# Kernel tuning notes

Hardware: AMD Instinct MI355X
Metric: run time of the kernel (lower is better)

## Reference

```python
import jax, jax.numpy as jnp
import numpy as np

NUM_HEADS = 8
D_HEAD = 64
LN_EPS = 1e-6


def _pad_idx(lengths, max_len):
    # flat indices into a [B*max_len, ...] dense buffer for each packed token
    return np.concatenate([b * max_len + np.arange(int(l)) for b, l in enumerate(lengths)])


def _layer_norm(x, scale, bias):
    mu = jnp.mean(x, axis=-1, keepdims=True)
    var = jnp.mean(jnp.square(x - mu), axis=-1, keepdims=True)
    return (x - mu) * jax.lax.rsqrt(var + LN_EPS) * scale + bias


def setup_inputs() -> dict:
    key = jax.random.key(0)
    ks = jax.random.split(key, 12)
    d_model, d_ff, H, dh = 512, 2048, NUM_HEADS, D_HEAD
    lengths = np.array([128 * (i + 1) for i in range(8)], dtype=np.int64)  # sum = 4608
    total = int(lengths.sum())
    s = 0.02
    return {
        "x": jax.random.normal(ks[0], (total, d_model), jnp.float32),
        "mem": jax.random.normal(ks[1], (total, d_model), jnp.float32),
        "lengths_x": lengths,
        "lengths_mem": lengths.copy(),
        "Wq": jax.random.normal(ks[2], (d_model, H * dh), jnp.float32) * s,
        "Wk": jax.random.normal(ks[3], (d_model, H * dh), jnp.float32) * s,
        "Wv": jax.random.normal(ks[4], (d_model, H * dh), jnp.float32) * s,
        "Wo": jax.random.normal(ks[5], (H * dh, d_model), jnp.float32) * s,
        "ln1_scale": jnp.ones((d_model,), jnp.float32),
        "ln1_bias": jnp.zeros((d_model,), jnp.float32),
        "W1": jax.random.normal(ks[6], (d_model, d_ff), jnp.float32) * s,
        "b1": jnp.zeros((d_ff,), jnp.float32),
        "W2": jax.random.normal(ks[7], (d_ff, d_model), jnp.float32) * s,
        "b2": jnp.zeros((d_model,), jnp.float32),
        "ln2_scale": jnp.ones((d_model,), jnp.float32),
        "ln2_bias": jnp.zeros((d_model,), jnp.float32),
    }


def reference(x, mem, lengths_x, lengths_mem, Wq, Wk, Wv, Wo,
              ln1_scale, ln1_bias, W1, b1, W2, b2, ln2_scale, ln2_bias):
    lx = np.asarray(lengths_x)
    lm = np.asarray(lengths_mem)
    B = lx.shape[0]
    Lx = int(lx.max())
    Lm = int(lm.max())
    H, dh = NUM_HEADS, D_HEAD

    idx_x = _pad_idx(lx, Lx)
    idx_m = _pad_idx(lm, Lm)

    def pad(packed, idx, B, L):
        dense = jnp.zeros((B * L,) + packed.shape[1:], packed.dtype).at[idx].set(packed)
        return dense.reshape((B, L) + packed.shape[1:])

    q = pad((x @ Wq).reshape(-1, H, dh), idx_x, B, Lx)   # [B, Lx, H, dh]
    k = pad((mem @ Wk).reshape(-1, H, dh), idx_m, B, Lm)  # [B, Lm, H, dh]
    v = pad((mem @ Wv).reshape(-1, H, dh), idx_m, B, Lm)

    e = jnp.einsum('bxhd,byhd->bhxy', q, k) / np.sqrt(dh)  # [B, H, Lx, Lm]
    # validity mask: (query pos < len_x) & (key pos < len_mem)
    mask = (np.arange(Lx)[None, :, None] < lx[:, None, None]) & \
           (np.arange(Lm)[None, None, :] < lm[:, None, None])
    mask = jnp.asarray(mask)[:, None, :, :]  # [B, 1, Lx, Lm]
    e = jnp.where(mask, e, jnp.float32(-1e30))  # finite -inf surrogate; identical softmax on valid rows
    alpha = jax.nn.softmax(e, axis=-1)
    out = jnp.einsum('bhxy,byhd->bxhd', alpha, v).reshape(B, Lx, H * dh)
    out = out @ Wo                                  # [B, Lx, d_model]
    out = out.reshape(B * Lx, -1)[idx_x]            # pack back to [total_x, d_model]

    h = _layer_norm(x + out, ln1_scale, ln1_bias)
    ffn = jax.nn.relu(h @ W1 + b1) @ W2 + b2
    return _layer_norm(h + ffn, ln2_scale, ln2_bias)
```

## Files before the change

### kernel.cpp

```cpp
#include <hip/hip_runtime.h>
#include <stdint.h>

typedef short bf8v __attribute__((ext_vector_type(8)));
typedef float f4v  __attribute__((ext_vector_type(4)));
typedef short s8v  __attribute__((ext_vector_type(8)));
typedef short s4v  __attribute__((ext_vector_type(4)));
typedef int   i2v  __attribute__((ext_vector_type(2)));

__device__ __forceinline__ float bf2f(short b){
  unsigned u = ((unsigned)(unsigned short)b) << 16;
  union { unsigned u; float f; } c; c.u = u; return c.f;
}
__device__ __forceinline__ short f2bf(float f){
  union { float f; unsigned u; } c; c.f = f;
  unsigned r = (c.u + 0x7FFFu + ((c.u >> 16) & 1u)) >> 16;
  return (short)r;
}
__device__ __forceinline__ void gload16(const short* g, short* l){
  __builtin_amdgcn_global_load_lds(
      (const __attribute__((address_space(1))) void*)g,
      (__attribute__((address_space(3))) void*)l, 16, 0, 0);
}

__global__ __launch_bounds__(256) void setup_kernel(
    const int* lx, const int* lm, int* meta,
    const float* __restrict__ x, const float* __restrict__ mem,
    short* __restrict__ xb, short* __restrict__ mb, long long n, int nblk_cvt,
    const float* __restrict__ Wq, const float* __restrict__ Wk,
    const float* __restrict__ Wv, const float* __restrict__ Wo,
    const float* __restrict__ W1, const float* __restrict__ W2,
    short* __restrict__ WqT, short* __restrict__ WkT,
    short* __restrict__ WvT, short* __restrict__ WoT,
    short* __restrict__ W1T, short* __restrict__ W2T){
  __shared__ int sjp[9], skvc[8];
  __shared__ float tile[32][33];
  int tid = threadIdx.x;
  int bid = blockIdx.x;

  if (bid == 0){
    if (tid == 0){
      int is64 = ((lx[1] | lx[3] | lx[5] | lx[7]) == 0) ? 1 : 0;
      int ox = 0, om = 0;
      for (int b = 0; b < 8; ++b){
        int a = is64 ? lx[2*b] : lx[b];
        int c = is64 ? lm[2*b] : lm[b];
        meta[b] = a; meta[8+b] = c;
        meta[16+b] = ox; meta[25+b] = om;
        ox += a; om += c;
      }
      meta[24] = ox; meta[33] = om;
      int jp = 0;
      for (int b = 0; b < 8; ++b){
        int Lm_ = meta[8+b];
        int kvc = (Lm_ + 255) / 256; if (kvc > 4) kvc = 4; if (kvc < 1) kvc = 1;
        int clen = (((Lm_ + kvc - 1) / kvc) + 31) & ~31;
        meta[34+b] = kvc; meta[42+b] = clen;
        meta[50+b] = jp;
        sjp[b] = jp; skvc[b] = kvc;
        int qt = (meta[b] + 63) / 64;
        jp += qt * kvc * 8;
      }
      meta[58] = jp;
      sjp[8] = jp;
    }
    __syncthreads();
    int njobs = sjp[8];
    for (int j = tid; j < njobs; j += blockDim.x){
      int b = 0;
      #pragma unroll
      for (int i = 1; i < 8; ++i) if (j >= sjp[i]) b = i;
      int local = j - sjp[b];
      int kvc = skvc[b];
      int h = local & 7;
      int r = local >> 3;
      int c = r % kvc;
      int qt = r / kvc;
      meta[64+j] = b | (h << 4) | (c << 7) | (qt << 11);
    }
    return;
  }

  if (bid <= nblk_cvt){
    long long t = (long long)(bid - 1) * 256 + tid;
    long long i = t * 8;
    const float* s; short* d;
    if (i < n){ s = x + i; d = xb + i; }
    else {
      i -= n; if (i >= n) return;
      s = mem + i; d = mb + i;
    }
    float4 f0 = *(const float4*)s;
    float4 f1 = *(const float4*)(s + 4);
    s8v o;
    o[0]=f2bf(f0.x); o[1]=f2bf(f0.y); o[2]=f2bf(f0.z); o[3]=f2bf(f0.w);
    o[4]=f2bf(f1.x); o[5]=f2bf(f1.y); o[6]=f2bf(f1.z); o[7]=f2bf(f1.w);
    *(s8v*)d = o;
    return;
  }

  int wbid = bid - 1 - nblk_cvt;
  const float* W; short* WT; int K, N, t0;
  if      (wbid <  256){ W=Wq; WT=WqT; K=512;  N=512;  t0=0;    }
  else if (wbid <  512){ W=Wk; WT=WkT; K=512;  N=512;  t0=256;  }
  else if (wbid <  768){ W=Wv; WT=WvT; K=512;  N=512;  t0=512;  }
  else if (wbid < 1024){ W=Wo; WT=WoT; K=512;  N=512;  t0=768;  }
  else if (wbid < 2048){ W=W1; WT=W1T; K=512;  N=2048; t0=1024; }
  else                 { W=W2; WT=W2T; K=2048; N=512;  t0=2048; }
  int lt = wbid - t0;
  int ntn = N / 32;
  int tk = lt / ntn, tn = lt % ntn;
  int r0 = tid >> 5, c = tid & 31;
  #pragma unroll
  for (int i = 0; i < 4; ++i){
    int r = r0 + i*8;
    tile[r][c] = W[(long)(tk*32 + r)*N + tn*32 + c];
  }
  __syncthreads();
  #pragma unroll
  for (int i = 0; i < 4; ++i){
    int r = r0 + i*8;
    WT[(long)(tn*32 + r)*K + tk*32 + c] = f2bf(tile[c][r]);
  }
}

__device__ __forceinline__ void stage_g64(const short* A, const short* Bt,
    long brow, long bcol, int M, int N, int K, int t,
    short* Als, short* Bls){
  int tid = threadIdx.x;
  {
    int cc = tid;
    int row = cc >> 2, slot = cc & 3;
    int cg = slot ^ ((row >> 1) & 3);
    long ar = brow + row; if (ar >= M) ar = M - 1;
    gload16(A + ar*(long)K + t + cg*8, &Als[cc*8]);
  }
  #pragma unroll
  for (int i = 0; i < 2; ++i){
    int cc = i*256 + tid;
    int row = cc >> 2, slot = cc & 3;
    int cg = slot ^ ((row >> 1) & 3);
    long br = bcol + row; if (br >= N) br = N - 1;
    gload16(Bt + br*(long)K + t + cg*8, &Bls[cc*8]);
  }
}

__device__ __forceinline__ void gemm_core64(const short* A, const short* Bt,
    short* __restrict__ Cb, const float* __restrict__ bias,
    int M, int N, int K, int k0, int klen,
    float scale, int relu, int colmajor,
    long brow, long bcol, short* Als, short* Bls){
  int tid = threadIdx.x;
  int lane = tid & 63, w = tid >> 6;
  int wcol = w * 32;
  int l15 = lane & 15, l4 = lane >> 4;

  f4v acc[4][2];
  #pragma unroll
  for (int m = 0; m < 4; ++m)
    #pragma unroll
    for (int n = 0; n < 2; ++n) acc[m][n] = (f4v){0.f,0.f,0.f,0.f};

  int nt = klen / 32;
  stage_g64(A, Bt, brow, bcol, M, N, K, k0, Als, Bls);
  for (int t = 0; t < nt; ++t){
    __syncthreads();
    if (t + 1 < nt)
      stage_g64(A, Bt, brow, bcol, M, N, K, k0 + (t+1)*32,
                Als + ((t+1)&1)*2048, Bls + ((t+1)&1)*4096);
    const short* Ab = Als + (t&1)*2048;
    const short* Bb = Bls + (t&1)*4096;
    bf8v a[4], b[2];
    #pragma unroll
    for (int m = 0; m < 4; ++m){
      int row = m*16 + l15;
      a[m] = *(const bf8v*)&Ab[row*32 + (l4 ^ ((row >> 1) & 3))*8];
    }
    #pragma unroll
    for (int n = 0; n < 2; ++n){
      int row = wcol + n*16 + l15;
      b[n] = *(const bf8v*)&Bb[row*32 + (l4 ^ ((row >> 1) & 3))*8];
    }
    #pragma unroll
    for (int m = 0; m < 4; ++m){
      acc[m][0] = __builtin_amdgcn_mfma_f32_16x16x32_bf16(a[m], b[0], acc[m][0], 0, 0, 0);
      acc[m][1] = __builtin_amdgcn_mfma_f32_16x16x32_bf16(a[m], b[1], acc[m][1], 0, 0, 0);
    }
  }

  #pragma unroll
  for (int m = 0; m < 4; ++m){
    #pragma unroll
    for (int n = 0; n < 2; ++n){
      long col = bcol + wcol + n*16 + l15;
      float bi = (bias != nullptr && col < N) ? bias[col] : 0.f;
      #pragma unroll
      for (int j = 0; j < 4; ++j){
        long row = brow + m*16 + 4*l4 + j;
        if (row < M && col < N){
          float v = acc[m][n][j] * scale + bi;
          if (relu) v = fmaxf(v, 0.f);
          Cb[colmajor ? (col*(long)M + row) : (row*(long)N + col)] = f2bf(v);
        }
      }
    }
  }
}

__global__ __launch_bounds__(256) void gemm64(
    const short* __restrict__ A, const short* __restrict__ Bt,
    short* __restrict__ C, const float* __restrict__ bias,
    int M, int N, int K, int klen, float scale, int relu, int colmajor){
  __shared__ __align__(16) short Als[2*64*32];
  __shared__ __align__(16) short Bls[2*128*32];
  int chunk = blockIdx.z;
  gemm_core64(A, Bt, C + (long)chunk * M * N, bias, M, N, K, chunk*klen, klen,
              scale, relu, colmajor,
              (long)blockIdx.y * 64, (long)blockIdx.x * 128, Als, Bls);
}

__global__ __launch_bounds__(256) void gemm_qkv(
    const short* __restrict__ xb, const short* __restrict__ mb,
    const short* __restrict__ WqT, const short* __restrict__ WkT,
    const short* __restrict__ WvT,
    short* __restrict__ Qb, short* __restrict__ Kbf, short* __restrict__ Vtb,
    int total){
  __shared__ __align__(16) short Als[2*64*32];
  __shared__ __align__(16) short Bls[2*128*32];
  int seg = blockIdx.x >> 2;
  const short* A  = (seg == 0) ? xb : mb;
  const short* Bt = (seg == 0) ? WqT : ((seg == 1) ? WkT : WvT);
  short* C        = (seg == 0) ? Qb  : ((seg == 1) ? Kbf : Vtb);
  float scale     = (seg == 0) ? 0.125f : 1.f;
  int colmajor    = (seg == 2);
  gemm_core64(A, Bt, C, nullptr, total, 512, 512, 0, 512, scale, 0, colmajor,
              (long)blockIdx.y * 64, (long)(blockIdx.x & 3) * 128, Als, Bls);
}

__global__ __launch_bounds__(256) void attn_kernel(
    const short* __restrict__ Q, const short* __restrict__ Kb,
    const short* __restrict__ Vt, short* __restrict__ Ob,
    short* __restrict__ Opart, float* __restrict__ mlpart,
    const int* __restrict__ meta, int total){
  __shared__ __align__(16) short Kls[2][32*64];
  __shared__ __align__(16) short Vls[2][64*32];
  __shared__ __align__(16) short Pls[4][16*32];
  int tid = threadIdx.x;
  int lane = tid & 63, w = tid >> 6;
  int l15 = lane & 15, l4 = lane >> 4;
  int njobs = meta[58];

  for (int j = blockIdx.x; j < njobs; j += gridDim.x){
    int word = meta[64+j];
    int b = word & 15, h = (word >> 4) & 7, c = (word >> 7) & 15, qt = word >> 11;
    int Lx = meta[b], Lm = meta[8+b];
    int ox = meta[16+b], om = meta[25+b];
    int kvc = meta[34+b], clen = meta[42+b];
    int c0 = c * clen;
    int cend = c0 + clen; if (cend > Lm) cend = Lm;
    int nt = (cend - c0 + 31) / 32;
    int qbase = qt*64 + w*16;

    __syncthreads();

    #define ATTN_STAGE(T, BUF)                                                  \
      {                                                                         \
        int kv0_ = c0 + (T)*32;                                                 \
        int kr = tid >> 3, ks_ = tid & 7;                                       \
        int cgk = ks_ ^ (kr & 7);                                               \
        int ktok = kv0_ + kr; if (ktok >= Lm) ktok = Lm - 1;                    \
        gload16(Kb + (long)(om + ktok)*512 + h*64 + cgk*8, &Kls[BUF][tid*8]);   \
        int vr = tid >> 2, vs = tid & 3;                                        \
        int cgv = vs ^ (vr & 3);                                                \
        int vkv = kv0_ + cgv*8; if (vkv + 8 > Lm) vkv = Lm - 8;                 \
        gload16(Vt + (long)(h*64 + vr)*total + om + vkv, &Vls[BUF][tid*8]);     \
      }

    ATTN_STAGE(0, 0)

    int qr = qbase + l15;
    const short* qp = Q + (long)(ox + (qr < Lx ? qr : Lx - 1))*512 + h*64 + l4*8;
    bf8v aq0 = *(const bf8v*)qp;
    bf8v aq1 = *(const bf8v*)(qp + 32);

    float mrun = -1e30f, lrun = 0.f;
    f4v o[4];
    #pragma unroll
    for (int n = 0; n < 4; ++n) o[n] = (f4v){0.f,0.f,0.f,0.f};

    for (int t = 0; t < nt; ++t){
      __syncthreads();
      if (t + 1 < nt) ATTN_STAGE(t+1, (t+1)&1)
      int buf = t & 1;
      int kv0 = c0 + t*32;

      f4v s[2];
      #pragma unroll
      for (int n = 0; n < 2; ++n){
        int krow = n*16 + l15;
        bf8v k0 = *(const bf8v*)&Kls[buf][krow*64 + ((l4    ) ^ (krow & 7))*8];
        bf8v k1 = *(const bf8v*)&Kls[buf][krow*64 + ((4 + l4) ^ (krow & 7))*8];
        f4v z = (f4v){0.f,0.f,0.f,0.f};
        z = __builtin_amdgcn_mfma_f32_16x16x32_bf16(k0, aq0, z, 0, 0, 0);
        z = __builtin_amdgcn_mfma_f32_16x16x32_bf16(k1, aq1, z, 0, 0, 0);
        s[n] = z;
      }
      if (kv0 + 32 > cend){
        #pragma unroll
        for (int n = 0; n < 2; ++n){
          int kvb = kv0 + n*16 + 4*l4;
          #pragma unroll
          for (int jj = 0; jj < 4; ++jj)
            if (kvb + jj >= cend) s[n][jj] = -1e30f;
        }
      }
      float m1 = fmaxf(fmaxf(fmaxf(s[0][0], s[0][1]), fmaxf(s[0][2], s[0][3])),
                       fmaxf(fmaxf(s[1][0], s[1][1]), fmaxf(s[1][2], s[1][3])));
      m1 = fmaxf(m1, __shfl_xor(m1, 16, 64));
      m1 = fmaxf(m1, __shfl_xor(m1, 32, 64));
      float mnew = fmaxf(mrun, m1);
      float sc = __expf(mrun - mnew);
      mrun = mnew;
      float rs = 0.f;
      #pragma unroll
      for (int n = 0; n < 2; ++n)
        #pragma unroll
        for (int jj = 0; jj < 4; ++jj){
          float p = __expf(s[n][jj] - mnew);
          s[n][jj] = p; rs += p;
        }
      rs += __shfl_xor(rs, 16, 64);
      rs += __shfl_xor(rs, 32, 64);
      lrun = lrun * sc + rs;
      #pragma unroll
      for (int n = 0; n < 4; ++n) o[n] *= sc;

      #pragma unroll
      for (int n = 0; n < 2; ++n){
        unsigned r0, r1;
        asm("v_cvt_pk_bf16_f32 %0, %1, %2" : "=v"(r0) : "v"(s[n][0]), "v"(s[n][1]));
        asm("v_cvt_pk_bf16_f32 %0, %1, %2" : "=v"(r1) : "v"(s[n][2]), "v"(s[n][3]));
        i2v pr; pr[0] = (int)r0; pr[1] = (int)r1;
        int cs = (n*4 + l4) ^ ((l15 & 3) << 1);
        *(i2v*)&Pls[w][l15*32 + cs*4] = pr;
      }
      bf8v pb = *(const bf8v*)&Pls[w][l15*32 + (((2*l4) ^ ((l15 & 3) << 1))*4)];

      #pragma unroll
      for (int n2 = 0; n2 < 4; ++n2){
        int vrow = n2*16 + l15;
        bf8v vv = *(const bf8v*)&Vls[buf][vrow*32 + ((l4 ^ (vrow & 3))*8)];
        o[n2] = __builtin_amdgcn_mfma_f32_16x16x32_bf16(vv, pb, o[n2], 0, 0, 0);
      }
    }
    #undef ATTN_STAGE

    if (qr < Lx){
      if (kvc == 1){
        float inv = 1.f / lrun;
        long obase = (long)(ox + qr)*512 + h*64;
        #pragma unroll
        for (int n2 = 0; n2 < 4; ++n2){
          s4v ov;
          #pragma unroll
          for (int jj = 0; jj < 4; ++jj) ov[jj] = f2bf(o[n2][jj] * inv);
          *(s4v*)&Ob[obase + n2*16 + l4*4] = ov;
        }
      } else {
        long slot = ((long)(ox + qr)*8 + h)*4 + c;
        #pragma unroll
        for (int n2 = 0; n2 < 4; ++n2){
          s4v ov;
          #pragma unroll
          for (int jj = 0; jj < 4; ++jj) ov[jj] = f2bf(o[n2][jj]);
          *(s4v*)&Opart[slot*64 + n2*16 + l4*4] = ov;
        }
        if (l4 == 0){
          float2 ml; ml.x = mrun; ml.y = lrun;
          *(float2*)&mlpart[slot*2] = ml;
        }
      }
    }
  }
}

__global__ __launch_bounds__(256) void attn_combine(
    const short* __restrict__ Opart, const float* __restrict__ mlpart,
    short* __restrict__ Ob, const int* __restrict__ meta, int total){
  int w = threadIdx.x >> 6, lane = threadIdx.x & 63;
  int row = blockIdx.x*4 + w;
  if (row >= total) return;
  int b = 0;
  #pragma unroll
  for (int i = 1; i < 8; ++i) if (row >= meta[16+i]) b = i;
  int kvc = meta[34+b];
  if (kvc <= 1) return;
  for (int h = 0; h < 8; ++h){
    long sbase = ((long)row*8 + h)*4;
    float m_ = -1e30f;
    for (int c = 0; c < kvc; ++c) m_ = fmaxf(m_, mlpart[(sbase+c)*2]);
    float num = 0.f, den = 0.f;
    for (int c = 0; c < kvc; ++c){
      float mc = mlpart[(sbase+c)*2];
      float lc = mlpart[(sbase+c)*2 + 1];
      float wgt = __expf(mc - m_);
      num += wgt * bf2f(Opart[(sbase+c)*64 + lane]);
      den += wgt * lc;
    }
    Ob[(long)row*512 + h*64 + lane] = f2bf(num / den);
  }
}

__global__ __launch_bounds__(256) void ln_fuse(
    const float* __restrict__ Af, const short* __restrict__ Ab,
    const short* __restrict__ PartB, int nparts, long pstride,
    const float* __restrict__ bias,
    const float* __restrict__ gamma, const float* __restrict__ beta,
    short* __restrict__ outb, float* __restrict__ outf, int rows){
  int w = threadIdx.x >> 6, lane = threadIdx.x & 63;
  long row = (long)blockIdx.x * 4 + w;
  if (row >= rows) return;
  int c0 = lane * 8;
  long base = row * 512 + c0;
  float v[8];
  if (Af){
    float4 f0 = *(const float4*)(Af + base);
    float4 f1 = *(const float4*)(Af + base + 4);
    v[0]=f0.x; v[1]=f0.y; v[2]=f0.z; v[3]=f0.w;
    v[4]=f1.x; v[5]=f1.y; v[6]=f1.z; v[7]=f1.w;
  } else {
    s8v a = *(const s8v*)(Ab + base);
    #pragma unroll
    for (int j = 0; j < 8; ++j) v[j] = bf2f(a[j]);
  }
  for (int c = 0; c < nparts; ++c){
    s8v pv = *(const s8v*)(PartB + c*pstride + base);
    #pragma unroll
    for (int j = 0; j < 8; ++j) v[j] += bf2f(pv[j]);
  }
  if (bias){
    #pragma unroll
    for (int j = 0; j < 8; ++j) v[j] += bias[c0 + j];
  }
  float sum = 0.f;
  #pragma unroll
  for (int j = 0; j < 8; ++j) sum += v[j];
  #pragma unroll
  for (int m = 1; m < 64; m <<= 1) sum += __shfl_xor(sum, m, 64);
  float mu = sum * (1.f/512.f);
  float q = 0.f;
  #pragma unroll
  for (int j = 0; j < 8; ++j){ float d = v[j] - mu; q += d*d; }
  #pragma unroll
  for (int m = 1; m < 64; m <<= 1) q += __shfl_xor(q, m, 64);
  float rs = rsqrtf(q * (1.f/512.f) + 1e-6f);
  float ov[8];
  #pragma unroll
  for (int j = 0; j < 8; ++j)
    ov[j] = (v[j] - mu) * rs * gamma[c0 + j] + beta[c0 + j];
  if (outb){
    s8v os;
    #pragma unroll
    for (int j = 0; j < 8; ++j) os[j] = f2bf(ov[j]);
    *(s8v*)(outb + base) = os;
  }
  if (outf){
    float4 f0 = {ov[0], ov[1], ov[2], ov[3]};
    float4 f1 = {ov[4], ov[5], ov[6], ov[7]};
    *(float4*)(outf + base) = f0;
    *(float4*)(outf + base + 4) = f1;
  }
}

extern "C" void kernel_launch(void* const* d_in, const int* in_sizes, int n_in,
                              void* d_out, int out_size, void* d_ws, size_t ws_size,
                              hipStream_t stream){
  (void)n_in; (void)out_size; (void)ws_size;
  const float* x   = (const float*)d_in[0];
  const float* mem = (const float*)d_in[1];
  const int*   lxr = (const int*)d_in[2];
  const int*   lmr = (const int*)d_in[3];
  const float* Wq  = (const float*)d_in[4];
  const float* Wk  = (const float*)d_in[5];
  const float* Wv  = (const float*)d_in[6];
  const float* Wo  = (const float*)d_in[7];
  const float* g1  = (const float*)d_in[8];
  const float* be1 = (const float*)d_in[9];
  const float* W1  = (const float*)d_in[10];
  const float* b1  = (const float*)d_in[11];
  const float* W2  = (const float*)d_in[12];
  const float* b2  = (const float*)d_in[13];
  const float* g2  = (const float*)d_in[14];
  const float* be2 = (const float*)d_in[15];
  float* out = (float*)d_out;

  int total = in_sizes[0] / 512;
  if (total <= 0) return;
  long long n = (long long)total * 512;

  char* p = (char*)d_ws;
  int*   meta  = (int*)p;    p += 16384;
  short* xb    = (short*)p;  p += n*2;
  short* mb    = (short*)p;  p += n*2;
  short* Qb    = (short*)p;  p += n*2;
  short* Kbf   = (short*)p;  p += n*2;
  short* Vtb   = (short*)p;  p += n*2;
  short* attnb = (short*)p;  p += n*2;
  short* hb    = (short*)p;  p += n*2;
  short* ffn1  = (short*)p;  p += (long long)total*2048*2;
  short* Opart = (short*)p;  p += (long long)total*8*4*64*2;
  float* mlprt = (float*)p;  p += (long long)total*8*4*2*4;
  short* p_wo  = (short*)p;  p += n*2*2;
  short* p_ff  = (short*)p;  p += n*4*2;
  short* WqT   = (short*)p;  p += 512*512*2;
  short* WkT   = (short*)p;  p += 512*512*2;
  short* WvT   = (short*)p;  p += 512*512*2;
  short* WoT   = (short*)p;  p += 512*512*2;
  short* W1T   = (short*)p;  p += 2048*512*2;
  short* W2T   = (short*)p;  p += 512*2048*2;

  int nblk_cvt = (int)(((2*n)/8 + 255) / 256);
  setup_kernel<<<dim3((unsigned)(1 + nblk_cvt + 3072)), 256, 0, stream>>>(
      lxr, lmr, meta, x, mem, xb, mb, n, nblk_cvt,
      Wq, Wk, Wv, Wo, W1, W2, WqT, WkT, WvT, WoT, W1T, W2T);

  int mt64 = (total + 63)/64;
  gemm_qkv<<<dim3(12, mt64), 256, 0, stream>>>(xb, mb, WqT, WkT, WvT, Qb, Kbf, Vtb, total);

  attn_kernel<<<dim3(2048), 256, 0, stream>>>(Qb, Kbf, Vtb, attnb,
                                              Opart, mlprt, meta, total);
  attn_combine<<<dim3((unsigned)((total + 3)/4)), 256, 0, stream>>>(
      Opart, mlprt, attnb, meta, total);

  gemm64<<<dim3(4, mt64, 2), 256, 0, stream>>>(attnb, WoT, p_wo, nullptr,
                                               total, 512, 512, 256, 1.f, 0, 0);
  ln_fuse<<<dim3((unsigned)((total + 3)/4)), 256, 0, stream>>>(
      x, nullptr, p_wo, 2, n, nullptr, g1, be1, hb, nullptr, total);

  gemm64<<<dim3(16, mt64, 1), 256, 0, stream>>>(hb, W1T, ffn1, b1,
                                                total, 2048, 512, 512, 1.f, 1, 0);
  gemm64<<<dim3(4, mt64, 4), 256, 0, stream>>>(ffn1, W2T, p_ff, nullptr,
                                               total, 512, 2048, 512, 1.f, 0, 0);
  ln_fuse<<<dim3((unsigned)((total + 3)/4)), 256, 0, stream>>>(
      nullptr, hb, p_ff, 4, n, b2, g2, be2, nullptr, out, total);
}
```

Measured before the change: 173.4 us.

## Fuse input bf16 conversion into QKV GEMM and split-K combine into attention

Removes the separate fp32-to-bf16 conversion of x and mem by having the QKV GEMM load fp32 rows and convert them while staging into LDS. Folds the split-KV combine into the attention kernel: the last block per (batch, q-tile, head) group, picked by an atomic counter, does the merge. Also raises the Wo GEMM split-K factor from 2 to 4. This saves two kernel launches and a round trip of bf16 copies, at the cost of synchronous fp32 loads in the QKV stage, fences and atomics in attention, and more partial sums for LayerNorm to read.

New measurement: 468.5 us. 2.7x slower.

```diff
diff --git a/kernel.cpp b/kernel.cpp
--- a/kernel.cpp
+++ b/kernel.cpp
@@ -24,8 +24,6 @@
 
 __global__ __launch_bounds__(256) void setup_kernel(
     const int* lx, const int* lm, int* meta,
-    const float* __restrict__ x, const float* __restrict__ mem,
-    short* __restrict__ xb, short* __restrict__ mb, long long n, int nblk_cvt,
     const float* __restrict__ Wq, const float* __restrict__ Wk,
     const float* __restrict__ Wv, const float* __restrict__ Wo,
     const float* __restrict__ W1, const float* __restrict__ W2,
@@ -77,28 +75,11 @@
       int qt = r / kvc;
       meta[64+j] = b | (h << 4) | (c << 7) | (qt << 11);
     }
+    for (int g = tid; g < 1024; g += blockDim.x) meta[2304 + g] = 0;
     return;
   }
 
-  if (bid <= nblk_cvt){
-    long long t = (long long)(bid - 1) * 256 + tid;
-    long long i = t * 8;
-    const float* s; short* d;
-    if (i < n){ s = x + i; d = xb + i; }
-    else {
-      i -= n; if (i >= n) return;
-      s = mem + i; d = mb + i;
-    }
-    float4 f0 = *(const float4*)s;
-    float4 f1 = *(const float4*)(s + 4);
-    s8v o;
-    o[0]=f2bf(f0.x); o[1]=f2bf(f0.y); o[2]=f2bf(f0.z); o[3]=f2bf(f0.w);
-    o[4]=f2bf(f1.x); o[5]=f2bf(f1.y); o[6]=f2bf(f1.z); o[7]=f2bf(f1.w);
-    *(s8v*)d = o;
-    return;
-  }
-
-  int wbid = bid - 1 - nblk_cvt;
+  int wbid = bid - 1;
   const float* W; short* WT; int K, N, t0;
   if      (wbid <  256){ W=Wq; WT=WqT; K=512;  N=512;  t0=0;    }
   else if (wbid <  512){ W=Wk; WT=WkT; K=512;  N=512;  t0=256;  }
@@ -123,16 +104,26 @@
   }
 }
 
-__device__ __forceinline__ void stage_g64(const short* A, const short* Bt,
+template<bool AF32>
+__device__ __forceinline__ void stage_g64(const void* A, const short* Bt,
     long brow, long bcol, int M, int N, int K, int t,
     short* Als, short* Bls){
   int tid = threadIdx.x;
   {
-    int cc = tid;
-    int row = cc >> 2, slot = cc & 3;
+    int row = tid >> 2, slot = tid & 3;
     int cg = slot ^ ((row >> 1) & 3);
     long ar = brow + row; if (ar >= M) ar = M - 1;
-    gload16(A + ar*(long)K + t + cg*8, &Als[cc*8]);
+    if constexpr (AF32){
+      const float* src = (const float*)A + ar*(long)K + t + cg*8;
+      float4 f0 = *(const float4*)src;
+      float4 f1 = *(const float4*)(src + 4);
+      s8v o;
+      o[0]=f2bf(f0.x); o[1]=f2bf(f0.y); o[2]=f2bf(f0.z); o[3]=f2bf(f0.w);
+      o[4]=f2bf(f1.x); o[5]=f2bf(f1.y); o[6]=f2bf(f1.z); o[7]=f2bf(f1.w);
+      *(s8v*)&Als[tid*8] = o;
+    } else {
+      gload16((const short*)A + ar*(long)K + t + cg*8, &Als[tid*8]);
+    }
   }
   #pragma unroll
   for (int i = 0; i < 2; ++i){
@@ -144,7 +135,8 @@
   }
 }
 
-__device__ __forceinline__ void gemm_core64(const short* A, const short* Bt,
+template<bool AF32>
+__device__ __forceinline__ void gemm_core64(const void* A, const short* Bt,
     short* __restrict__ Cb, const float* __restrict__ bias,
     int M, int N, int K, int k0, int klen,
     float scale, int relu, int colmajor,
@@ -161,12 +153,12 @@
     for (int n = 0; n < 2; ++n) acc[m][n] = (f4v){0.f,0.f,0.f,0.f};
 
   int nt = klen / 32;
-  stage_g64(A, Bt, brow, bcol, M, N, K, k0, Als, Bls);
+  stage_g64<AF32>(A, Bt, brow, bcol, M, N, K, k0, Als, Bls);
   for (int t = 0; t < nt; ++t){
     __syncthreads();
     if (t + 1 < nt)
-      stage_g64(A, Bt, brow, bcol, M, N, K, k0 + (t+1)*32,
-                Als + ((t+1)&1)*2048, Bls + ((t+1)&1)*4096);
+      stage_g64<AF32>(A, Bt, brow, bcol, M, N, K, k0 + (t+1)*32,
+                      Als + ((t+1)&1)*2048, Bls + ((t+1)&1)*4096);
     const short* Ab = Als + (t&1)*2048;
     const short* Bb = Bls + (t&1)*4096;
     bf8v a[4], b[2];
@@ -213,13 +205,13 @@
   __shared__ __align__(16) short Als[2*64*32];
   __shared__ __align__(16) short Bls[2*128*32];
   int chunk = blockIdx.z;
-  gemm_core64(A, Bt, C + (long)chunk * M * N, bias, M, N, K, chunk*klen, klen,
-              scale, relu, colmajor,
-              (long)blockIdx.y * 64, (long)blockIdx.x * 128, Als, Bls);
+  gemm_core64<false>(A, Bt, C + (long)chunk * M * N, bias, M, N, K, chunk*klen, klen,
+                     scale, relu, colmajor,
+                     (long)blockIdx.y * 64, (long)blockIdx.x * 128, Als, Bls);
 }
 
 __global__ __launch_bounds__(256) void gemm_qkv(
-    const short* __restrict__ xb, const short* __restrict__ mb,
+    const float* __restrict__ x, const float* __restrict__ mem,
     const short* __restrict__ WqT, const short* __restrict__ WkT,
     const short* __restrict__ WvT,
     short* __restrict__ Qb, short* __restrict__ Kbf, short* __restrict__ Vtb,
@@ -227,23 +219,24 @@
   __shared__ __align__(16) short Als[2*64*32];
   __shared__ __align__(16) short Bls[2*128*32];
   int seg = blockIdx.x >> 2;
-  const short* A  = (seg == 0) ? xb : mb;
+  const float* A  = (seg == 0) ? x : mem;
   const short* Bt = (seg == 0) ? WqT : ((seg == 1) ? WkT : WvT);
   short* C        = (seg == 0) ? Qb  : ((seg == 1) ? Kbf : Vtb);
   float scale     = (seg == 0) ? 0.125f : 1.f;
   int colmajor    = (seg == 2);
-  gemm_core64(A, Bt, C, nullptr, total, 512, 512, 0, 512, scale, 0, colmajor,
-              (long)blockIdx.y * 64, (long)(blockIdx.x & 3) * 128, Als, Bls);
+  gemm_core64<true>(A, Bt, C, nullptr, total, 512, 512, 0, 512, scale, 0, colmajor,
+                    (long)blockIdx.y * 64, (long)(blockIdx.x & 3) * 128, Als, Bls);
 }
 
 __global__ __launch_bounds__(256) void attn_kernel(
     const short* __restrict__ Q, const short* __restrict__ Kb,
     const short* __restrict__ Vt, short* __restrict__ Ob,
     short* __restrict__ Opart, float* __restrict__ mlpart,
-    const int* __restrict__ meta, int total){
+    const int* __restrict__ meta, int* __restrict__ cnt, int total){
   __shared__ __align__(16) short Kls[2][32*64];
   __shared__ __align__(16) short Vls[2][64*32];
   __shared__ __align__(16) short Pls[4][16*32];
+  __shared__ int slast;
   int tid = threadIdx.x;
   int lane = tid & 63, w = tid >> 6;
   int l15 = lane & 15, l4 = lane >> 4;
@@ -380,33 +373,37 @@
         }
       }
     }
-  }
-}
-
-__global__ __launch_bounds__(256) void attn_combine(
-    const short* __restrict__ Opart, const float* __restrict__ mlpart,
-    short* __restrict__ Ob, const int* __restrict__ meta, int total){
-  int w = threadIdx.x >> 6, lane = threadIdx.x & 63;
-  int row = blockIdx.x*4 + w;
-  if (row >= total) return;
-  int b = 0;
-  #pragma unroll
-  for (int i = 1; i < 8; ++i) if (row >= meta[16+i]) b = i;
-  int kvc = meta[34+b];
-  if (kvc <= 1) return;
-  for (int h = 0; h < 8; ++h){
-    long sbase = ((long)row*8 + h)*4;
-    float m_ = -1e30f;
-    for (int c = 0; c < kvc; ++c) m_ = fmaxf(m_, mlpart[(sbase+c)*2]);
-    float num = 0.f, den = 0.f;
-    for (int c = 0; c < kvc; ++c){
-      float mc = mlpart[(sbase+c)*2];
-      float lc = mlpart[(sbase+c)*2 + 1];
-      float wgt = __expf(mc - m_);
-      num += wgt * bf2f(Opart[(sbase+c)*64 + lane]);
-      den += wgt * lc;
-    }
-    Ob[(long)row*512 + h*64 + lane] = f2bf(num / den);
+
+    if (kvc > 1){
+      __threadfence();
+      __syncthreads();
+      if (tid == 0){
+        int g = ((b*16 + qt) << 3) + h;
+        int old = atomicAdd(&cnt[g], 1);
+        slast = (old == kvc - 1) ? 1 : 0;
+      }
+      __syncthreads();
+      if (slast){
+        __threadfence();
+        for (int rr = w; rr < 64; rr += 4){
+          int row = qt*64 + rr;
+          if (row < Lx){
+            long sbase = ((long)(ox + row)*8 + h)*4;
+            float m_ = -1e30f;
+            for (int c2 = 0; c2 < kvc; ++c2) m_ = fmaxf(m_, mlpart[(sbase+c2)*2]);
+            float num = 0.f, den = 0.f;
+            for (int c2 = 0; c2 < kvc; ++c2){
+              float mc = mlpart[(sbase+c2)*2];
+              float lc = mlpart[(sbase+c2)*2 + 1];
+              float wgt = __expf(mc - m_);
+              num += wgt * bf2f(Opart[(sbase+c2)*64 + lane]);
+              den += wgt * lc;
+            }
+            Ob[(long)(ox + row)*512 + h*64 + lane] = f2bf(num / den);
+          }
+        }
+      }
+    }
   }
 }
 
@@ -499,8 +496,6 @@
 
   char* p = (char*)d_ws;
   int*   meta  = (int*)p;    p += 16384;
-  short* xb    = (short*)p;  p += n*2;
-  short* mb    = (short*)p;  p += n*2;
   short* Qb    = (short*)p;  p += n*2;
   short* Kbf   = (short*)p;  p += n*2;
   short* Vtb   = (short*)p;  p += n*2;
@@ -509,7 +504,7 @@
   short* ffn1  = (short*)p;  p += (long long)total*2048*2;
   short* Opart = (short*)p;  p += (long long)total*8*4*64*2;
   float* mlprt = (float*)p;  p += (long long)total*8*4*2*4;
-  short* p_wo  = (short*)p;  p += n*2*2;
+  short* p_wo  = (short*)p;  p += n*4*2;
   short* p_ff  = (short*)p;  p += n*4*2;
   short* WqT   = (short*)p;  p += 512*512*2;
   short* WkT   = (short*)p;  p += 512*512*2;
@@ -518,23 +513,21 @@
   short* W1T   = (short*)p;  p += 2048*512*2;
   short* W2T   = (short*)p;  p += 512*2048*2;
 
-  int nblk_cvt = (int)(((2*n)/8 + 255) / 256);
-  setup_kernel<<<dim3((unsigned)(1 + nblk_cvt + 3072)), 256, 0, stream>>>(
-      lxr, lmr, meta, x, mem, xb, mb, n, nblk_cvt,
-      Wq, Wk, Wv, Wo, W1, W2, WqT, WkT, WvT, WoT, W1T, W2T);
+  setup_kernel<<<dim3(1 + 3072), 256, 0, stream>>>(
+      lxr, lmr, meta, Wq, Wk, Wv, Wo, W1, W2, WqT, WkT, WvT, WoT, W1T, W2T);
 
   int mt64 = (total + 63)/64;
-  gemm_qkv<<<dim3(12, mt64), 256, 0, stream>>>(xb, mb, WqT, WkT, WvT, Qb, Kbf, Vtb, total);
+  gemm_qkv<<<dim3(12, mt64), 256, 0, stream>>>(x, mem, WqT, WkT, WvT,
+                                               Qb, Kbf, Vtb, total);
 
   attn_kernel<<<dim3(2048), 256, 0, stream>>>(Qb, Kbf, Vtb, attnb,
-                                              Opart, mlprt, meta, total);
-  attn_combine<<<dim3((unsigned)((total + 3)/4)), 256, 0, stream>>>(
-      Opart, mlprt, attnb, meta, total);
-
-  gemm64<<<dim3(4, mt64, 2), 256, 0, stream>>>(attnb, WoT, p_wo, nullptr,
-                                               total, 512, 512, 256, 1.f, 0, 0);
+                                              Opart, mlprt, meta,
+                                              meta + 2304, total);
+
+  gemm64<<<dim3(4, mt64, 4), 256, 0, stream>>>(attnb, WoT, p_wo, nullptr,
+                                               total, 512, 512, 128, 1.f, 0, 0);
   ln_fuse<<<dim3((unsigned)((total + 3)/4)), 256, 0, stream>>>(
-      x, nullptr, p_wo, 2, n, nullptr, g1, be1, hb, nullptr, total);
+      x, nullptr, p_wo, 4, n, nullptr, g1, be1, hb, nullptr, total);
 
   gemm64<<<dim3(16, mt64, 1), 256, 0, stream>>>(hb, W1T, ffn1, b1,
                                                 total, 2048, 512, 512, 1.f, 1, 0);
```
